# Kernel tuning notes

Hardware: AMD Instinct MI355X
Metric: run time of the kernel (lower is better)

The kernel has to match this reference:

```python
import jax, jax.numpy as jnp
import numpy as np

P_DIMS = [512, 256, 128]
K_DIMS = [256, 256, 256]
NT = 65536


def setup_inputs() -> dict:
    key = jax.random.key(0)
    ks = jax.random.split(key, 8 * len(P_DIMS))
    inp = {}
    ki = 0
    for i, (p, k) in enumerate(zip(P_DIMS, K_DIMS)):
        inp[f"x{i}"] = jax.random.normal(ks[ki], (NT, p), jnp.float32); ki += 1
        inp[f"alpha{i}"] = jax.random.normal(ks[ki], (1, k), jnp.float32); ki += 1
        inp[f"beta{i}"] = jax.random.normal(ks[ki], (k, p), jnp.float32) * 0.05; ki += 1
        inp[f"sig{i}"] = jax.random.normal(ks[ki], (1, k), jnp.float32); ki += 1
        inp[f"eta{i}"] = jax.random.normal(ks[ki], (1, k), jnp.float32); ki += 1
        inp[f"gam{i}"] = jax.random.normal(ks[ki], (k, 1), jnp.float32) * 0.03; ki += 1
        inp[f"w{i}"] = jax.random.normal(ks[ki], (k, p), jnp.float32); ki += 1
        inp[f"disc{i}"] = jnp.array([3.0], jnp.float32); ki += 1
    return inp


def _source(x, alpha, beta, sig, eta, gam, w, disc):
    # x: (nt,p); w,beta: (k,p); alpha,sig,eta: (1,k); gam: (k,1); disc: (1,)
    h = eta ** 2                                           # (1,k)
    d2 = (jnp.sum(x * x, axis=1, keepdims=True)
          - 2.0 * (x @ w.T)
          + jnp.sum(w * w, axis=1)[None, :])
    a = jnp.exp(-(gam[:, 0] ** 2)[None, :] * d2)           # (nt,k)
    ah = a * h                                             # a * H
    hx = jnp.sum(ah, axis=1)                               # (nt,)
    mu = x @ beta.T + alpha                                # (nt,k)
    mux = jnp.sum(mu * ah, axis=1) / hx
    sig2x = jnp.sum((sig ** 2) * (ah ** 2), axis=1) / (hx * hx)
    hx_dc = hx * jax.nn.sigmoid(disc[0])
    return mux, sig2x, hx, hx_dc


def reference(x0, alpha0, beta0, sig0, eta0, gam0, w0, disc0,
              x1, alpha1, beta1, sig1, eta1, gam1, w1, disc1,
              x2, alpha2, beta2, sig2, eta2, gam2, w2, disc2):
    srcs = [
        (x0, alpha0, beta0, sig0, eta0, gam0, w0, disc0),
        (x1, alpha1, beta1, sig1, eta1, gam1, w1, disc1),
        (x2, alpha2, beta2, sig2, eta2, gam2, w2, disc2),
    ]
    outs = [_source(*s) for s in srcs]  # fixed small loop over sources
    mux_t = jnp.stack([o[0] for o in outs])     # (S,nt)
    sig2x_t = jnp.stack([o[1] for o in outs])
    hx_t = jnp.stack([o[2] for o in outs])
    hx_dc = jnp.stack([o[3] for o in outs])
    denom = jnp.sum(hx_dc, axis=0)
    mux_comb = jnp.sum(mux_t * hx_dc, axis=0) / denom
    sig2x_comb = jnp.sum(sig2x_t * hx_dc ** 2, axis=0) / (denom ** 2)
    mux_final = jnp.concatenate([mux_t, mux_comb[None]], axis=0)      # (S+1,nt)
    sig2x_final = jnp.concatenate([sig2x_t, sig2x_comb[None]], axis=0)
    hx_final = jnp.concatenate([hx_t, denom[None]], axis=0)
    return (mux_final, sig2x_final, hx_final)
```

## Files before the change

kernel.cpp:

```cpp
#include <hip/hip_runtime.h>
#include <hip/hip_bf16.h>

typedef __attribute__((ext_vector_type(8))) short short8;
typedef __attribute__((ext_vector_type(4))) float f32x4;

#define NT 65536

__device__ __forceinline__ unsigned short f2bf(float f) {
    union { float f; unsigned int u; } v; v.f = f;
    unsigned int u = v.u;
    unsigned int r = (u + 0x7fffu + ((u >> 16) & 1u)) >> 16;
    return (unsigned short)r;
}

__device__ __forceinline__ unsigned int cvt_pk_bf16(float lo, float hi) {
    unsigned int r;
    asm("v_cvt_pk_bf16_f32 %0, %1, %2" : "=v"(r) : "v"(lo), "v"(hi));
    return r;
}

__global__ void prep_kernel(const float* __restrict__ w, const float* __restrict__ beta,
                            const float* __restrict__ alpha, const float* __restrict__ sig,
                            const float* __restrict__ eta, const float* __restrict__ gam,
                            unsigned short* __restrict__ bc, float* __restrict__ prm, int P) {
    __shared__ float red[2];
    const int n = blockIdx.x;
    const int tid = threadIdx.x;
    const int wb = n >> 5;
    const int j = n & 31;
    const bool isw = (j < 16);
    const int k = wb * 16 + (j & 15);
    const float* src = (isw ? w : beta) + (size_t)k * P;
    unsigned short* dst = bc + (size_t)n * P;
    float ss = 0.f;
    for (int c = tid; c < P; c += 128) {
        float f = src[c];
        dst[c] = f2bf(f);
        if (isw) ss += f * f;
    }
#pragma unroll
    for (int m = 1; m < 64; m <<= 1) ss += __shfl_xor(ss, m);
    if ((tid & 63) == 0) red[tid >> 6] = ss;
    __syncthreads();
    if (isw && tid == 0) prm[k] = red[0] + red[1];
    if (n == 0) {
        for (int kk = tid; kk < 256; kk += 128) {
            float g = gam[kk], e = eta[kk];
            prm[256 + kk]  = g * g;
            prm[512 + kk]  = e * e;
            prm[768 + kk]  = alpha[kk];
            prm[1024 + kk] = sig[kk] * sig[kk];
        }
    }
}

template<int P>
__global__ __launch_bounds__(512, 2)
void fused_src(const float* __restrict__ x, const unsigned short* __restrict__ Bc,
               const float* __restrict__ prm, float* __restrict__ pws) {
    constexpr int KS  = P / 32;
    constexpr int IST = P / 64;
    constexpr int WIN = (P == 256) ? 4 : 2;
    __shared__ unsigned short As[2][64 * P];
    __shared__ float part[8][64][3];
    __shared__ float xn2s[2][64];

    const int bx = blockIdx.x;
    const int h  = bx & 1;
    const int rg = bx >> 1;
    const int tid = threadIdx.x, lane = tid & 63, wv = tid >> 6;
    const int l15 = lane & 15, l4 = lane >> 4;
    const int wb = h * 8 + wv;

    short8 Bf[2][KS];
#pragma unroll
    for (int st = 0; st < 2; st++)
#pragma unroll
        for (int ks = 0; ks < KS; ks++)
            Bf[st][ks] = *(const short8*)(Bc + (size_t)(wb * 32 + st * 16 + l15) * P + ks * 32 + l4 * 8);

    const int kb = wb * 16 + 4 * l4;
    const f32x4 wn2 = *(const f32x4*)(prm + kb);
    const f32x4 g2  = *(const f32x4*)(prm + 256 + kb);
    const f32x4 hv  = *(const f32x4*)(prm + 512 + kb);
    const f32x4 alv = *(const f32x4*)(prm + 768 + kb);
    const f32x4 s2v = *(const f32x4*)(prm + 1024 + kb);

    float* pw = pws + (size_t)h * 3 * NT;

    const int srow = tid >> 3;
    const int ssl0 = tid & 7;

    {
        const int row0 = rg * 64;
        float4 pa[IST], pb[IST];
#pragma unroll
        for (int i = 0; i < IST; i++) {
            const float* gp = x + (size_t)(row0 + srow) * P + (ssl0 + 8 * i) * 8;
            pa[i] = *(const float4*)(gp);
            pb[i] = *(const float4*)(gp + 4);
        }
        float ssacc = 0.f;
#pragma unroll
        for (int i = 0; i < IST; i++) {
            float4 a0 = pa[i], a1 = pb[i];
            ssacc += a0.x*a0.x + a0.y*a0.y + a0.z*a0.z + a0.w*a0.w
                   + a1.x*a1.x + a1.y*a1.y + a1.z*a1.z + a1.w*a1.w;
            uint4 pk = { cvt_pk_bf16(a0.x, a0.y), cvt_pk_bf16(a0.z, a0.w),
                         cvt_pk_bf16(a1.x, a1.y), cvt_pk_bf16(a1.z, a1.w) };
            const int slot = ssl0 + 8 * i;
            *(uint4*)(&As[0][srow * P + ((slot ^ (srow & 7)) << 3)]) = pk;
        }
        ssacc += __shfl_xor(ssacc, 1);
        ssacc += __shfl_xor(ssacc, 2);
        ssacc += __shfl_xor(ssacc, 4);
        if (ssl0 == 0) xn2s[0][srow] = ssacc;
    }
    __syncthreads();

    int buf = 0;
    for (int tt = 0; tt < 8; tt++) {
        const int tile = rg + 128 * tt;
        const int row0 = tile * 64;
        const bool more = (tt < 7);
        const int nrow0 = (tile + 128) * 64;

        f32x4 acc[2][4];
#pragma unroll
        for (int st = 0; st < 2; st++)
#pragma unroll
            for (int rf = 0; rf < 4; rf++) acc[st][rf] = (f32x4){0.f, 0.f, 0.f, 0.f};

        float4 gfa[WIN], gfb[WIN];
        float ssacc = 0.f;

#pragma unroll
        for (int ks = 0; ks < KS; ks++) {
            if (more && ks >= WIN && (ks - WIN) < IST) {
                const int i = ks - WIN;
                float4 a0 = gfa[i % WIN], a1 = gfb[i % WIN];
                ssacc += a0.x*a0.x + a0.y*a0.y + a0.z*a0.z + a0.w*a0.w
                       + a1.x*a1.x + a1.y*a1.y + a1.z*a1.z + a1.w*a1.w;
                uint4 pk = { cvt_pk_bf16(a0.x, a0.y), cvt_pk_bf16(a0.z, a0.w),
                             cvt_pk_bf16(a1.x, a1.y), cvt_pk_bf16(a1.z, a1.w) };
                const int slot = ssl0 + 8 * i;
                *(uint4*)(&As[buf ^ 1][srow * P + ((slot ^ (srow & 7)) << 3)]) = pk;
            }
            if (more && ks < IST) {
                const float* gp = x + (size_t)(nrow0 + srow) * P + (ssl0 + 8 * ks) * 8;
                gfa[ks % WIN] = *(const float4*)(gp);
                gfb[ks % WIN] = *(const float4*)(gp + 4);
            }
            short8 af[4];
#pragma unroll
            for (int rf = 0; rf < 4; rf++) {
                const int row = 16 * rf + l15;
                af[rf] = *(const short8*)(&As[buf][row * P + (((ks * 4 + l4) ^ (row & 7)) << 3)]);
            }
#pragma unroll
            for (int rf = 0; rf < 4; rf++) {
                acc[0][rf] = __builtin_amdgcn_mfma_f32_16x16x32_bf16(Bf[0][ks], af[rf], acc[0][rf], 0, 0, 0);
                acc[1][rf] = __builtin_amdgcn_mfma_f32_16x16x32_bf16(Bf[1][ks], af[rf], acc[1][rf], 0, 0, 0);
            }
        }

        if (more) {
            ssacc += __shfl_xor(ssacc, 1);
            ssacc += __shfl_xor(ssacc, 2);
            ssacc += __shfl_xor(ssacc, 4);
            if (ssl0 == 0) xn2s[buf ^ 1][srow] = ssacc;
        }

#pragma unroll
        for (int rf = 0; rf < 4; rf++) {
            const int row = 16 * rf + l15;
            const float xv = xn2s[buf][row];
            float hs = 0.f, ms = 0.f, gs = 0.f;
#pragma unroll
            for (int j = 0; j < 4; j++) {
                float d2 = xv - 2.f * acc[0][rf][j] + wn2[j];
                float a  = __expf(-g2[j] * d2);
                float ah = a * hv[j];
                hs += ah;
                ms += (acc[1][rf][j] + alv[j]) * ah;
                gs += s2v[j] * ah * ah;
            }
            hs += __shfl_xor(hs, 16); hs += __shfl_xor(hs, 32);
            ms += __shfl_xor(ms, 16); ms += __shfl_xor(ms, 32);
            gs += __shfl_xor(gs, 16); gs += __shfl_xor(gs, 32);
            if (l4 == 0) { part[wv][row][0] = hs; part[wv][row][1] = ms; part[wv][row][2] = gs; }
        }
        __syncthreads();
        if (tid < 192) {
            const int v = tid >> 6, r = tid & 63;
            float sum = 0.f;
#pragma unroll
            for (int w8 = 0; w8 < 8; w8++) sum += part[w8][r][v];
            pw[(size_t)v * NT + row0 + r] = sum;
        }
        __syncthreads();
        buf ^= 1;
    }
}

__global__ void combine_kernel(const float* __restrict__ pws,
                               const float* __restrict__ d0, const float* __restrict__ d1,
                               const float* __restrict__ d2, float* __restrict__ out) {
    const int t = blockIdx.x * 256 + threadIdx.x;
    float mux[3], s2x[3], hx[3];
#pragma unroll
    for (int s = 0; s < 3; s++) {
        const float* b = pws + (size_t)s * 6 * NT;
        const float hh = b[t] + b[(size_t)3 * NT + t];
        const float mm = b[(size_t)1 * NT + t] + b[(size_t)4 * NT + t];
        const float gg = b[(size_t)2 * NT + t] + b[(size_t)5 * NT + t];
        mux[s] = mm / hh; s2x[s] = gg / (hh * hh); hx[s] = hh;
        out[(size_t)s * NT + t]       = mux[s];
        out[(size_t)(4 + s) * NT + t] = s2x[s];
        out[(size_t)(8 + s) * NT + t] = hh;
    }
    const float sd0 = 1.f / (1.f + __expf(-d0[0]));
    const float sd1 = 1.f / (1.f + __expf(-d1[0]));
    const float sd2 = 1.f / (1.f + __expf(-d2[0]));
    const float c0 = hx[0] * sd0, c1 = hx[1] * sd1, c2 = hx[2] * sd2;
    const float den = c0 + c1 + c2;
    const float muc = mux[0] * c0 + mux[1] * c1 + mux[2] * c2;
    const float sgc = s2x[0] * c0 * c0 + s2x[1] * c1 * c1 + s2x[2] * c2 * c2;
    out[(size_t)3 * NT + t]  = muc / den;
    out[(size_t)7 * NT + t]  = sgc / (den * den);
    out[(size_t)11 * NT + t] = den;
}

extern "C" void kernel_launch(void* const* d_in, const int* in_sizes, int n_in,
                              void* d_out, int out_size, void* d_ws, size_t ws_size,
                              hipStream_t stream) {
    const float* x0 = (const float*)d_in[0];
    const float* x1 = (const float*)d_in[8];
    const float* x2 = (const float*)d_in[16];

    unsigned short* bc = (unsigned short*)d_ws;
    float* prmAll = (float*)((char*)d_ws + 917504);
    float* pws    = (float*)((char*)d_ws + 917504 + 15360);
    float* out = (float*)d_out;

    const int Ps[3] = {512, 256, 128};
    const size_t bcoff[3] = {0, 512 * 512, 512 * 512 + 512 * 256};
    for (int s = 0; s < 3; s++) {
        prep_kernel<<<512, 128, 0, stream>>>((const float*)d_in[8 * s + 6], (const float*)d_in[8 * s + 2],
                                             (const float*)d_in[8 * s + 1], (const float*)d_in[8 * s + 3],
                                             (const float*)d_in[8 * s + 4], (const float*)d_in[8 * s + 5],
                                             bc + bcoff[s], prmAll + s * 1280, Ps[s]);
    }
    fused_src<512><<<256, 512, 0, stream>>>(x0, bc + bcoff[0], prmAll,          pws);
    fused_src<256><<<256, 512, 0, stream>>>(x1, bc + bcoff[1], prmAll + 1280,   pws + (size_t)6 * NT);
    fused_src<128><<<256, 512, 0, stream>>>(x2, bc + bcoff[2], prmAll + 2560,   pws + (size_t)12 * NT);
    combine_kernel<<<256, 256, 0, stream>>>(pws, (const float*)d_in[7], (const float*)d_in[15],
                                            (const float*)d_in[23], out);
}
```

Measured before the change: 133.9 us.

## Split P=512 reduction across wave pairs and widen k-split to four groups

For the P=512 source, each k-group of 16 columns is now handled by two waves, each covering half the reduction dimension. The two partial accumulators are summed through an LDS exchange that reuses the current A buffer. This halves the per-wave B fragment registers for P=512, and blocks are split four ways over k instead of two, giving more tiles per block with fewer row groups. The combine kernel now sums a variable number of partial groups per source. In exchange there is an extra barrier and LDS round-trip per tile, and half the waves sit idle during the epilogue.

New measurement: 149.5 us. 11.6% more time.

```diff
diff --git a/kernel.cpp b/kernel.cpp
--- a/kernel.cpp
+++ b/kernel.cpp
@@ -26,10 +26,10 @@
     __shared__ float red[2];
     const int n = blockIdx.x;
     const int tid = threadIdx.x;
-    const int wb = n >> 5;
-    const int j = n & 31;
-    const bool isw = (j < 16);
-    const int k = wb * 16 + (j & 15);
+    const int k16 = n >> 5;
+    const int typ = (n >> 4) & 1;
+    const int k = k16 * 16 + (n & 15);
+    const bool isw = (typ == 0);
     const float* src = (isw ? w : beta) + (size_t)k * P;
     unsigned short* dst = bc + (size_t)n * P;
     float ss = 0.f;
@@ -58,52 +58,55 @@
 __global__ __launch_bounds__(512, 2)
 void fused_src(const float* __restrict__ x, const unsigned short* __restrict__ Bc,
                const float* __restrict__ prm, float* __restrict__ pws) {
-    constexpr int KS  = P / 32;
-    constexpr int IST = P / 64;
-    constexpr int WIN = (P == 256) ? 4 : 2;
+    constexpr int  KSPLIT = (P == 512) ? 4 : 2;
+    constexpr bool PPS    = (P == 512);
+    constexpr int  KSW    = PPS ? P / 64 : P / 32;
+    constexpr int  IST    = P / 64;
+    constexpr int  WIN    = (IST < 4) ? IST : 4;
+    constexpr int  NRG    = 256 / KSPLIT;
+    constexpr int  T      = 1024 / NRG;
+
     __shared__ unsigned short As[2][64 * P];
+    __shared__ float xn2s[2][64];
     __shared__ float part[8][64][3];
-    __shared__ float xn2s[2][64];
 
     const int bx = blockIdx.x;
-    const int h  = bx & 1;
-    const int rg = bx >> 1;
+    const int h  = bx / NRG;
+    const int rg = bx % NRG;
     const int tid = threadIdx.x, lane = tid & 63, wv = tid >> 6;
     const int l15 = lane & 15, l4 = lane >> 4;
-    const int wb = h * 8 + wv;
-
-    short8 Bf[2][KS];
-#pragma unroll
-    for (int st = 0; st < 2; st++)
-#pragma unroll
-        for (int ks = 0; ks < KS; ks++)
-            Bf[st][ks] = *(const short8*)(Bc + (size_t)(wb * 32 + st * 16 + l15) * P + ks * 32 + l4 * 8);
-
-    const int kb = wb * 16 + 4 * l4;
+
+    int k16, pp, kset;
+    if (PPS) { kset = wv >> 1; pp = wv & 1; k16 = h * 4 + kset; }
+    else     { kset = wv;      pp = 0;      k16 = h * 8 + wv; }
+    const int ppoff = PPS ? pp * (P / 2) : 0;
+
+    short8 Bf[2][KSW];
+#pragma unroll
+    for (int typ = 0; typ < 2; typ++)
+#pragma unroll
+        for (int ks = 0; ks < KSW; ks++)
+            Bf[typ][ks] = *(const short8*)(Bc + (size_t)(k16 * 32 + typ * 16 + l15) * P
+                                           + ppoff + ks * 32 + l4 * 8);
+
+    const int kb = k16 * 16 + 4 * l4;
     const f32x4 wn2 = *(const f32x4*)(prm + kb);
     const f32x4 g2  = *(const f32x4*)(prm + 256 + kb);
     const f32x4 hv  = *(const f32x4*)(prm + 512 + kb);
     const f32x4 alv = *(const f32x4*)(prm + 768 + kb);
     const f32x4 s2v = *(const f32x4*)(prm + 1024 + kb);
 
-    float* pw = pws + (size_t)h * 3 * NT;
-
     const int srow = tid >> 3;
     const int ssl0 = tid & 7;
 
     {
         const int row0 = rg * 64;
-        float4 pa[IST], pb[IST];
+        float ssacc = 0.f;
 #pragma unroll
         for (int i = 0; i < IST; i++) {
             const float* gp = x + (size_t)(row0 + srow) * P + (ssl0 + 8 * i) * 8;
-            pa[i] = *(const float4*)(gp);
-            pb[i] = *(const float4*)(gp + 4);
-        }
-        float ssacc = 0.f;
-#pragma unroll
-        for (int i = 0; i < IST; i++) {
-            float4 a0 = pa[i], a1 = pb[i];
+            float4 a0 = *(const float4*)(gp);
+            float4 a1 = *(const float4*)(gp + 4);
             ssacc += a0.x*a0.x + a0.y*a0.y + a0.z*a0.z + a0.w*a0.w
                    + a1.x*a1.x + a1.y*a1.y + a1.z*a1.z + a1.w*a1.w;
             uint4 pk = { cvt_pk_bf16(a0.x, a0.y), cvt_pk_bf16(a0.z, a0.w),
@@ -119,28 +122,27 @@
     __syncthreads();
 
     int buf = 0;
-    for (int tt = 0; tt < 8; tt++) {
-        const int tile = rg + 128 * tt;
-        const int row0 = tile * 64;
-        const bool more = (tt < 7);
-        const int nrow0 = (tile + 128) * 64;
+    for (int tt = 0; tt < T; tt++) {
+        const int row0 = (rg + NRG * tt) * 64;
+        const bool more = (tt < T - 1);
+        const int nrow0 = (rg + NRG * (tt + 1)) * 64;
 
         f32x4 acc[2][4];
 #pragma unroll
-        for (int st = 0; st < 2; st++)
-#pragma unroll
-            for (int rf = 0; rf < 4; rf++) acc[st][rf] = (f32x4){0.f, 0.f, 0.f, 0.f};
-
-        float4 gfa[WIN], gfb[WIN];
-        float ssacc = 0.f;
-
-#pragma unroll
-        for (int ks = 0; ks < KS; ks++) {
+        for (int typ = 0; typ < 2; typ++)
+#pragma unroll
+            for (int rf = 0; rf < 4; rf++) acc[typ][rf] = (f32x4){0.f, 0.f, 0.f, 0.f};
+
+        float4 ga[WIN], gb[WIN];
+        float ssn = 0.f;
+
+#pragma unroll
+        for (int ks = 0; ks < KSW; ks++) {
             if (more && ks >= WIN && (ks - WIN) < IST) {
                 const int i = ks - WIN;
-                float4 a0 = gfa[i % WIN], a1 = gfb[i % WIN];
-                ssacc += a0.x*a0.x + a0.y*a0.y + a0.z*a0.z + a0.w*a0.w
-                       + a1.x*a1.x + a1.y*a1.y + a1.z*a1.z + a1.w*a1.w;
+                float4 a0 = ga[i % WIN], a1 = gb[i % WIN];
+                ssn += a0.x*a0.x + a0.y*a0.y + a0.z*a0.z + a0.w*a0.w
+                     + a1.x*a1.x + a1.y*a1.y + a1.z*a1.z + a1.w*a1.w;
                 uint4 pk = { cvt_pk_bf16(a0.x, a0.y), cvt_pk_bf16(a0.z, a0.w),
                              cvt_pk_bf16(a1.x, a1.y), cvt_pk_bf16(a1.z, a1.w) };
                 const int slot = ssl0 + 8 * i;
@@ -148,14 +150,15 @@
             }
             if (more && ks < IST) {
                 const float* gp = x + (size_t)(nrow0 + srow) * P + (ssl0 + 8 * ks) * 8;
-                gfa[ks % WIN] = *(const float4*)(gp);
-                gfb[ks % WIN] = *(const float4*)(gp + 4);
+                ga[ks % WIN] = *(const float4*)(gp);
+                gb[ks % WIN] = *(const float4*)(gp + 4);
             }
             short8 af[4];
 #pragma unroll
             for (int rf = 0; rf < 4; rf++) {
                 const int row = 16 * rf + l15;
-                af[rf] = *(const short8*)(&As[buf][row * P + (((ks * 4 + l4) ^ (row & 7)) << 3)]);
+                const int slotIdx = (ppoff >> 3) + ks * 4 + l4;
+                af[rf] = *(const short8*)(&As[buf][row * P + ((slotIdx ^ (row & 7)) << 3)]);
             }
 #pragma unroll
             for (int rf = 0; rf < 4; rf++) {
@@ -165,40 +168,75 @@
         }
 
         if (more) {
-            ssacc += __shfl_xor(ssacc, 1);
-            ssacc += __shfl_xor(ssacc, 2);
-            ssacc += __shfl_xor(ssacc, 4);
-            if (ssl0 == 0) xn2s[buf ^ 1][srow] = ssacc;
-        }
-
-#pragma unroll
-        for (int rf = 0; rf < 4; rf++) {
-            const int row = 16 * rf + l15;
-            const float xv = xn2s[buf][row];
-            float hs = 0.f, ms = 0.f, gs = 0.f;
-#pragma unroll
-            for (int j = 0; j < 4; j++) {
-                float d2 = xv - 2.f * acc[0][rf][j] + wn2[j];
-                float a  = __expf(-g2[j] * d2);
-                float ah = a * hv[j];
-                hs += ah;
-                ms += (acc[1][rf][j] + alv[j]) * ah;
-                gs += s2v[j] * ah * ah;
-            }
-            hs += __shfl_xor(hs, 16); hs += __shfl_xor(hs, 32);
-            ms += __shfl_xor(ms, 16); ms += __shfl_xor(ms, 32);
-            gs += __shfl_xor(gs, 16); gs += __shfl_xor(gs, 32);
-            if (l4 == 0) { part[wv][row][0] = hs; part[wv][row][1] = ms; part[wv][row][2] = gs; }
+#pragma unroll
+            for (int i = (KSW - WIN < 0 ? 0 : KSW - WIN); i < IST; i++) {
+                float4 a0 = ga[i % WIN], a1 = gb[i % WIN];
+                ssn += a0.x*a0.x + a0.y*a0.y + a0.z*a0.z + a0.w*a0.w
+                     + a1.x*a1.x + a1.y*a1.y + a1.z*a1.z + a1.w*a1.w;
+                uint4 pk = { cvt_pk_bf16(a0.x, a0.y), cvt_pk_bf16(a0.z, a0.w),
+                             cvt_pk_bf16(a1.x, a1.y), cvt_pk_bf16(a1.z, a1.w) };
+                const int slot = ssl0 + 8 * i;
+                *(uint4*)(&As[buf ^ 1][srow * P + ((slot ^ (srow & 7)) << 3)]) = pk;
+            }
+            ssn += __shfl_xor(ssn, 1);
+            ssn += __shfl_xor(ssn, 2);
+            ssn += __shfl_xor(ssn, 4);
+            if (ssl0 == 0) xn2s[buf ^ 1][srow] = ssn;
         }
         __syncthreads();
+
+        if constexpr (PPS) {
+            f32x4* exch = (f32x4*)&As[buf][0];
+            if (pp == 1) {
+#pragma unroll
+                for (int typ = 0; typ < 2; typ++)
+#pragma unroll
+                    for (int rf = 0; rf < 4; rf++)
+                        exch[((kset * 2 + typ) * 4 + rf) * 64 + lane] = acc[typ][rf];
+            }
+            __syncthreads();
+            if (pp == 0) {
+#pragma unroll
+                for (int typ = 0; typ < 2; typ++)
+#pragma unroll
+                    for (int rf = 0; rf < 4; rf++) {
+                        f32x4 o = exch[((kset * 2 + typ) * 4 + rf) * 64 + lane];
+                        acc[typ][rf] += o;
+                    }
+            }
+        }
+
+        if (!PPS || pp == 0) {
+#pragma unroll
+            for (int rf = 0; rf < 4; rf++) {
+                const int row = 16 * rf + l15;
+                const float xv = xn2s[buf][row];
+                float hs = 0.f, ms = 0.f, gs = 0.f;
+#pragma unroll
+                for (int j = 0; j < 4; j++) {
+                    float d2 = xv - 2.f * acc[0][rf][j] + wn2[j];
+                    float a  = __expf(-g2[j] * d2);
+                    float ah = a * hv[j];
+                    hs += ah;
+                    ms += (acc[1][rf][j] + alv[j]) * ah;
+                    gs += s2v[j] * ah * ah;
+                }
+                hs += __shfl_xor(hs, 16); hs += __shfl_xor(hs, 32);
+                ms += __shfl_xor(ms, 16); ms += __shfl_xor(ms, 32);
+                gs += __shfl_xor(gs, 16); gs += __shfl_xor(gs, 32);
+                if (l4 == 0) { part[kset][row][0] = hs; part[kset][row][1] = ms; part[kset][row][2] = gs; }
+            }
+        }
+        __syncthreads();
+
         if (tid < 192) {
+            constexpr int NG = PPS ? 4 : 8;
             const int v = tid >> 6, r = tid & 63;
             float sum = 0.f;
 #pragma unroll
-            for (int w8 = 0; w8 < 8; w8++) sum += part[w8][r][v];
-            pw[(size_t)v * NT + row0 + r] = sum;
-        }
-        __syncthreads();
+            for (int g = 0; g < NG; g++) sum += part[g][r][v];
+            pws[(size_t)(h * 3 + v) * NT + row0 + r] = sum;
+        }
         buf ^= 1;
     }
 }
@@ -207,13 +245,18 @@
                                const float* __restrict__ d0, const float* __restrict__ d1,
                                const float* __restrict__ d2, float* __restrict__ out) {
     const int t = blockIdx.x * 256 + threadIdx.x;
+    const int ng[3]  = {4, 2, 2};
+    const int off[3] = {0, 12, 18};
     float mux[3], s2x[3], hx[3];
 #pragma unroll
     for (int s = 0; s < 3; s++) {
-        const float* b = pws + (size_t)s * 6 * NT;
-        const float hh = b[t] + b[(size_t)3 * NT + t];
-        const float mm = b[(size_t)1 * NT + t] + b[(size_t)4 * NT + t];
-        const float gg = b[(size_t)2 * NT + t] + b[(size_t)5 * NT + t];
+        const float* b = pws + (size_t)off[s] * NT;
+        float hh = 0.f, mm = 0.f, gg = 0.f;
+        for (int g = 0; g < ng[s]; g++) {
+            hh += b[(size_t)(g * 3 + 0) * NT + t];
+            mm += b[(size_t)(g * 3 + 1) * NT + t];
+            gg += b[(size_t)(g * 3 + 2) * NT + t];
+        }
         mux[s] = mm / hh; s2x[s] = gg / (hh * hh); hx[s] = hh;
         out[(size_t)s * NT + t]       = mux[s];
         out[(size_t)(4 + s) * NT + t] = s2x[s];
@@ -251,9 +294,9 @@
                                              (const float*)d_in[8 * s + 4], (const float*)d_in[8 * s + 5],
                                              bc + bcoff[s], prmAll + s * 1280, Ps[s]);
     }
-    fused_src<512><<<256, 512, 0, stream>>>(x0, bc + bcoff[0], prmAll,          pws);
-    fused_src<256><<<256, 512, 0, stream>>>(x1, bc + bcoff[1], prmAll + 1280,   pws + (size_t)6 * NT);
-    fused_src<128><<<256, 512, 0, stream>>>(x2, bc + bcoff[2], prmAll + 2560,   pws + (size_t)12 * NT);
+    fused_src<512><<<256, 512, 0, stream>>>(x0, bc + bcoff[0], prmAll,        pws);
+    fused_src<256><<<256, 512, 0, stream>>>(x1, bc + bcoff[1], prmAll + 1280, pws + (size_t)12 * NT);
+    fused_src<128><<<256, 512, 0, stream>>>(x2, bc + bcoff[2], prmAll + 2560, pws + (size_t)18 * NT);
     combine_kernel<<<256, 256, 0, stream>>>(pws, (const float*)d_in[7], (const float*)d_in[15],
                                             (const float*)d_in[23], out);
 }
```

## Fuse per-source launches into single 256x256-tile kernel with LDS-staged weights

Applied to the files above, without the earlier changes.

Merges the three prep launches and the three per-source GEMM launches into one launch each, indexing the source by block ID. The main kernel switches from register-resident weight fragments with 64-row tiles to 256x256 output tiles with a K loop. Weights stream into double-buffered LDS via global_load_lds, while x is converted to bf16 in registers. The aim is to raise data reuse per tile and cut launch overhead and serialisation between sources. In exchange it needs about 150KB of LDS and a large accumulator, so only one block fits per CU, and the sources with shorter K have few loop iterations to overlap loads with compute.

After: 181.8 us. 1.36x slower.

```diff
diff --git a/kernel.cpp b/kernel.cpp
--- a/kernel.cpp
+++ b/kernel.cpp
@@ -19,19 +19,42 @@
     return r;
 }
 
-__global__ void prep_kernel(const float* __restrict__ w, const float* __restrict__ beta,
-                            const float* __restrict__ alpha, const float* __restrict__ sig,
-                            const float* __restrict__ eta, const float* __restrict__ gam,
-                            unsigned short* __restrict__ bc, float* __restrict__ prm, int P) {
+#define LGKM0() asm volatile("s_waitcnt lgkmcnt(0)" ::: "memory")
+#define VMC0()  asm volatile("s_waitcnt vmcnt(0)" ::: "memory")
+#define BAR()   __builtin_amdgcn_s_barrier()
+#define SB0()   __builtin_amdgcn_sched_barrier(0)
+
+__global__ void prep_kernel(const float* __restrict__ w0, const float* __restrict__ b0,
+                            const float* __restrict__ a0, const float* __restrict__ s0,
+                            const float* __restrict__ e0, const float* __restrict__ g0,
+                            const float* __restrict__ w1, const float* __restrict__ b1,
+                            const float* __restrict__ a1, const float* __restrict__ s1,
+                            const float* __restrict__ e1, const float* __restrict__ g1,
+                            const float* __restrict__ w2, const float* __restrict__ b2,
+                            const float* __restrict__ a2, const float* __restrict__ s2,
+                            const float* __restrict__ e2, const float* __restrict__ g2,
+                            unsigned short* __restrict__ bc, float* __restrict__ prmAll) {
     __shared__ float red[2];
-    const int n = blockIdx.x;
+    const int bx = blockIdx.x;
+    const int s = bx >> 9;
+    const int n = bx & 511;
+    const int P = 512 >> s;
+    const float* w   = (s == 0) ? w0 : ((s == 1) ? w1 : w2);
+    const float* bet = (s == 0) ? b0 : ((s == 1) ? b1 : b2);
+    const float* alp = (s == 0) ? a0 : ((s == 1) ? a1 : a2);
+    const float* sig = (s == 0) ? s0 : ((s == 1) ? s1 : s2);
+    const float* eta = (s == 0) ? e0 : ((s == 1) ? e1 : e2);
+    const float* gam = (s == 0) ? g0 : ((s == 1) ? g1 : g2);
+    unsigned short* dstb = bc + ((s == 0) ? 0 : ((s == 1) ? (512 * 512) : (512 * 512 + 512 * 256)));
+    float* prm = prmAll + 1280 * s;
+
     const int tid = threadIdx.x;
-    const int wb = n >> 5;
-    const int j = n & 31;
-    const bool isw = (j < 16);
-    const int k = wb * 16 + (j & 15);
-    const float* src = (isw ? w : beta) + (size_t)k * P;
-    unsigned short* dst = bc + (size_t)n * P;
+    const int k16 = n >> 5;
+    const int typ = (n >> 4) & 1;
+    const int k = k16 * 16 + (n & 15);
+    const bool isw = (typ == 0);
+    const float* src = (isw ? w : bet) + (size_t)k * P;
+    unsigned short* dst = dstb + (size_t)n * P;
     float ss = 0.f;
     for (int c = tid; c < P; c += 128) {
         float f = src[c];
@@ -48,158 +71,171 @@
             float g = gam[kk], e = eta[kk];
             prm[256 + kk]  = g * g;
             prm[512 + kk]  = e * e;
-            prm[768 + kk]  = alpha[kk];
+            prm[768 + kk]  = alp[kk];
             prm[1024 + kk] = sig[kk] * sig[kk];
         }
     }
 }
 
-template<int P>
 __global__ __launch_bounds__(512, 2)
-void fused_src(const float* __restrict__ x, const unsigned short* __restrict__ Bc,
-               const float* __restrict__ prm, float* __restrict__ pws) {
-    constexpr int KS  = P / 32;
-    constexpr int IST = P / 64;
-    constexpr int WIN = (P == 256) ? 4 : 2;
-    __shared__ unsigned short As[2][64 * P];
-    __shared__ float part[8][64][3];
-    __shared__ float xn2s[2][64];
+void fused_all(const float* __restrict__ x0, const float* __restrict__ x1, const float* __restrict__ x2,
+               const unsigned short* __restrict__ bcAll, const float* __restrict__ prmAll,
+               float* __restrict__ pws) {
+    __shared__ unsigned short Ab[2][256 * 72];
+    __shared__ unsigned short Bb[2][256 * 64];
+    __shared__ float xn2[256];
+    __shared__ float part[4][256][3];
 
     const int bx = blockIdx.x;
-    const int h  = bx & 1;
-    const int rg = bx >> 1;
+    const int s  = bx >> 9;
+    const int local = bx & 511;
+    const int mt = local & 255;
+    const int h  = local >> 8;
+    const int P  = 512 >> s;
+    const int NK = P >> 6;
+    const float* x = (s == 0) ? x0 : ((s == 1) ? x1 : x2);
+    const unsigned short* Bc = bcAll + ((s == 0) ? 0 : ((s == 1) ? (512 * 512) : (512 * 512 + 512 * 256)));
+    const float* prm = prmAll + 1280 * s;
+    float* pw = pws + (size_t)(s * 6 + h * 3) * NT;
+    const int row0 = mt * 256;
+
     const int tid = threadIdx.x, lane = tid & 63, wv = tid >> 6;
+    const int wr = wv >> 2, wcn = wv & 3;
     const int l15 = lane & 15, l4 = lane >> 4;
-    const int wb = h * 8 + wv;
-
-    short8 Bf[2][KS];
-#pragma unroll
-    for (int st = 0; st < 2; st++)
-#pragma unroll
-        for (int ks = 0; ks < KS; ks++)
-            Bf[st][ks] = *(const short8*)(Bc + (size_t)(wb * 32 + st * 16 + l15) * P + ks * 32 + l4 * 8);
-
-    const int kb = wb * 16 + 4 * l4;
-    const f32x4 wn2 = *(const f32x4*)(prm + kb);
-    const f32x4 g2  = *(const f32x4*)(prm + 256 + kb);
-    const f32x4 hv  = *(const f32x4*)(prm + 512 + kb);
-    const f32x4 alv = *(const f32x4*)(prm + 768 + kb);
-    const f32x4 s2v = *(const f32x4*)(prm + 1024 + kb);
-
-    float* pw = pws + (size_t)h * 3 * NT;
-
-    const int srow = tid >> 3;
-    const int ssl0 = tid & 7;
-
-    {
-        const int row0 = rg * 64;
-        float4 pa[IST], pb[IST];
-#pragma unroll
-        for (int i = 0; i < IST; i++) {
-            const float* gp = x + (size_t)(row0 + srow) * P + (ssl0 + 8 * i) * 8;
-            pa[i] = *(const float4*)(gp);
-            pb[i] = *(const float4*)(gp + 4);
-        }
-        float ssacc = 0.f;
-#pragma unroll
-        for (int i = 0; i < IST; i++) {
-            float4 a0 = pa[i], a1 = pb[i];
-            ssacc += a0.x*a0.x + a0.y*a0.y + a0.z*a0.z + a0.w*a0.w
-                   + a1.x*a1.x + a1.y*a1.y + a1.z*a1.z + a1.w*a1.w;
-            uint4 pk = { cvt_pk_bf16(a0.x, a0.y), cvt_pk_bf16(a0.z, a0.w),
-                         cvt_pk_bf16(a1.x, a1.y), cvt_pk_bf16(a1.z, a1.w) };
-            const int slot = ssl0 + 8 * i;
-            *(uint4*)(&As[0][srow * P + ((slot ^ (srow & 7)) << 3)]) = pk;
-        }
-        ssacc += __shfl_xor(ssacc, 1);
-        ssacc += __shfl_xor(ssacc, 2);
-        ssacc += __shfl_xor(ssacc, 4);
-        if (ssl0 == 0) xn2s[0][srow] = ssacc;
-    }
+
+    const int arow = tid >> 1, ahalf = tid & 1;
+    const float* xrow = x + (size_t)(row0 + arow) * P + ahalf * 32;
+
+    const int brr = tid >> 3;
+    const int bslot = (tid & 7) ^ (brr & 7);
+
+    f32x4 acc[8][4];
+#pragma unroll
+    for (int rf = 0; rf < 8; rf++)
+#pragma unroll
+        for (int cf = 0; cf < 4; cf++) acc[rf][cf] = (f32x4){0.f, 0.f, 0.f, 0.f};
+
+    float ss = 0.f;
+    float4 ar[8];
+
+    auto stage_B = [&](int nb, int t) {
+#pragma unroll
+        for (int i = 0; i < 4; i++) {
+            const unsigned short* src = Bc + (size_t)(256 * h + i * 64 + brr) * P + t * 64 + bslot * 8;
+            __builtin_amdgcn_global_load_lds((const __attribute__((address_space(1))) void*)src,
+                                             (__attribute__((address_space(3))) void*)&Bb[nb][(i * 512 + wv * 64) * 8],
+                                             16, 0, 0);
+        }
+    };
+    auto load_A = [&](int t) {
+#pragma unroll
+        for (int i = 0; i < 8; i++) ar[i] = *(const float4*)(xrow + t * 64 + i * 4);
+    };
+    auto cvt_write_A = [&](int nb) {
+#pragma unroll
+        for (int i2 = 0; i2 < 4; i2++) {
+            float4 q0 = ar[2 * i2], q1 = ar[2 * i2 + 1];
+            ss += q0.x*q0.x + q0.y*q0.y + q0.z*q0.z + q0.w*q0.w
+                + q1.x*q1.x + q1.y*q1.y + q1.z*q1.z + q1.w*q1.w;
+            uint4 pk = { cvt_pk_bf16(q0.x, q0.y), cvt_pk_bf16(q0.z, q0.w),
+                         cvt_pk_bf16(q1.x, q1.y), cvt_pk_bf16(q1.z, q1.w) };
+            *(uint4*)(&Ab[nb][arow * 72 + (ahalf * 4 + i2) * 8]) = pk;
+        }
+    };
+    auto compute = [&](int buf) {
+#pragma unroll
+        for (int kk = 0; kk < 2; kk++) {
+            short8 bfr[4];
+#pragma unroll
+            for (int cf = 0; cf < 4; cf++) {
+                const int rowb = wcn * 64 + cf * 16 + l15;
+                bfr[cf] = *(const short8*)(&Bb[buf][rowb * 64 + (((kk * 4 + l4) ^ (rowb & 7)) << 3)]);
+            }
+#pragma unroll
+            for (int rf = 0; rf < 8; rf++) {
+                const int rowa = wr * 128 + rf * 16 + l15;
+                short8 af = *(const short8*)(&Ab[buf][rowa * 72 + (kk * 4 + l4) * 8]);
+#pragma unroll
+                for (int cf = 0; cf < 4; cf++)
+                    acc[rf][cf] = __builtin_amdgcn_mfma_f32_16x16x32_bf16(af, bfr[cf], acc[rf][cf], 0, 0, 0);
+            }
+        }
+    };
+
+    stage_B(0, 0);
+    SB0();
+    load_A(0);
+    SB0();
+    cvt_write_A(0);
+    VMC0(); LGKM0(); BAR(); SB0();
+
+#pragma unroll 1
+    for (int t = 0; t < NK - 1; t++) {
+        const int buf = t & 1;
+        stage_B(buf ^ 1, t + 1);
+        SB0();
+        load_A(t + 1);
+        SB0();
+        compute(buf);
+        SB0();
+        cvt_write_A(buf ^ 1);
+        LGKM0(); BAR(); SB0();
+    }
+    compute((NK - 1) & 1);
+    VMC0(); LGKM0(); BAR(); SB0();
+
+    ss += __shfl_xor(ss, 1);
+    if (ahalf == 0) xn2[arow] = ss;
     __syncthreads();
 
-    int buf = 0;
-    for (int tt = 0; tt < 8; tt++) {
-        const int tile = rg + 128 * tt;
-        const int row0 = tile * 64;
-        const bool more = (tt < 7);
-        const int nrow0 = (tile + 128) * 64;
-
-        f32x4 acc[2][4];
-#pragma unroll
-        for (int st = 0; st < 2; st++)
-#pragma unroll
-            for (int rf = 0; rf < 4; rf++) acc[st][rf] = (f32x4){0.f, 0.f, 0.f, 0.f};
-
-        float4 gfa[WIN], gfb[WIN];
-        float ssacc = 0.f;
-
-#pragma unroll
-        for (int ks = 0; ks < KS; ks++) {
-            if (more && ks >= WIN && (ks - WIN) < IST) {
-                const int i = ks - WIN;
-                float4 a0 = gfa[i % WIN], a1 = gfb[i % WIN];
-                ssacc += a0.x*a0.x + a0.y*a0.y + a0.z*a0.z + a0.w*a0.w
-                       + a1.x*a1.x + a1.y*a1.y + a1.z*a1.z + a1.w*a1.w;
-                uint4 pk = { cvt_pk_bf16(a0.x, a0.y), cvt_pk_bf16(a0.z, a0.w),
-                             cvt_pk_bf16(a1.x, a1.y), cvt_pk_bf16(a1.z, a1.w) };
-                const int slot = ssl0 + 8 * i;
-                *(uint4*)(&As[buf ^ 1][srow * P + ((slot ^ (srow & 7)) << 3)]) = pk;
-            }
-            if (more && ks < IST) {
-                const float* gp = x + (size_t)(nrow0 + srow) * P + (ssl0 + 8 * ks) * 8;
-                gfa[ks % WIN] = *(const float4*)(gp);
-                gfb[ks % WIN] = *(const float4*)(gp + 4);
-            }
-            short8 af[4];
-#pragma unroll
-            for (int rf = 0; rf < 4; rf++) {
-                const int row = 16 * rf + l15;
-                af[rf] = *(const short8*)(&As[buf][row * P + (((ks * 4 + l4) ^ (row & 7)) << 3)]);
-            }
-#pragma unroll
-            for (int rf = 0; rf < 4; rf++) {
-                acc[0][rf] = __builtin_amdgcn_mfma_f32_16x16x32_bf16(Bf[0][ks], af[rf], acc[0][rf], 0, 0, 0);
-                acc[1][rf] = __builtin_amdgcn_mfma_f32_16x16x32_bf16(Bf[1][ks], af[rf], acc[1][rf], 0, 0, 0);
-            }
-        }
-
-        if (more) {
-            ssacc += __shfl_xor(ssacc, 1);
-            ssacc += __shfl_xor(ssacc, 2);
-            ssacc += __shfl_xor(ssacc, 4);
-            if (ssl0 == 0) xn2s[buf ^ 1][srow] = ssacc;
-        }
-
-#pragma unroll
-        for (int rf = 0; rf < 4; rf++) {
-            const int row = 16 * rf + l15;
-            const float xv = xn2s[buf][row];
+    float wn2q[2], g2q[2], hvq[2], alq[2], s2q[2];
+#pragma unroll
+    for (int q = 0; q < 2; q++) {
+        const int k = (8 * h + 2 * wcn + q) * 16 + l15;
+        wn2q[q] = prm[k];
+        g2q[q]  = prm[256 + k];
+        hvq[q]  = prm[512 + k];
+        alq[q]  = prm[768 + k];
+        s2q[q]  = prm[1024 + k];
+    }
+#pragma unroll
+    for (int rf = 0; rf < 8; rf++) {
+#pragma unroll
+        for (int j = 0; j < 4; j++) {
+            const int row = wr * 128 + rf * 16 + l4 * 4 + j;
+            const float xv = xn2[row];
             float hs = 0.f, ms = 0.f, gs = 0.f;
 #pragma unroll
-            for (int j = 0; j < 4; j++) {
-                float d2 = xv - 2.f * acc[0][rf][j] + wn2[j];
-                float a  = __expf(-g2[j] * d2);
-                float ah = a * hv[j];
+            for (int q = 0; q < 2; q++) {
+                const float aw = acc[rf][2 * q][j];
+                const float ab2 = acc[rf][2 * q + 1][j];
+                const float d2 = xv - 2.f * aw + wn2q[q];
+                const float a  = __expf(-g2q[q] * d2);
+                const float ah = a * hvq[q];
                 hs += ah;
-                ms += (acc[1][rf][j] + alv[j]) * ah;
-                gs += s2v[j] * ah * ah;
-            }
-            hs += __shfl_xor(hs, 16); hs += __shfl_xor(hs, 32);
-            ms += __shfl_xor(ms, 16); ms += __shfl_xor(ms, 32);
-            gs += __shfl_xor(gs, 16); gs += __shfl_xor(gs, 32);
-            if (l4 == 0) { part[wv][row][0] = hs; part[wv][row][1] = ms; part[wv][row][2] = gs; }
-        }
-        __syncthreads();
-        if (tid < 192) {
-            const int v = tid >> 6, r = tid & 63;
-            float sum = 0.f;
-#pragma unroll
-            for (int w8 = 0; w8 < 8; w8++) sum += part[w8][r][v];
-            pw[(size_t)v * NT + row0 + r] = sum;
-        }
-        __syncthreads();
-        buf ^= 1;
+                ms += (ab2 + alq[q]) * ah;
+                gs += s2q[q] * ah * ah;
+            }
+#pragma unroll
+            for (int msk = 1; msk < 16; msk <<= 1) {
+                hs += __shfl_xor(hs, msk);
+                ms += __shfl_xor(ms, msk);
+                gs += __shfl_xor(gs, msk);
+            }
+            if (l15 == 0) {
+                part[wcn][row][0] = hs;
+                part[wcn][row][1] = ms;
+                part[wcn][row][2] = gs;
+            }
+        }
+    }
+    __syncthreads();
+    if (tid < 256) {
+#pragma unroll
+        for (int v = 0; v < 3; v++) {
+            float sum = part[0][tid][v] + part[1][tid][v] + part[2][tid][v] + part[3][tid][v];
+            pw[(size_t)v * NT + row0 + tid] = sum;
+        }
     }
 }
 
@@ -243,17 +279,15 @@
     float* pws    = (float*)((char*)d_ws + 917504 + 15360);
     float* out = (float*)d_out;
 
-    const int Ps[3] = {512, 256, 128};
-    const size_t bcoff[3] = {0, 512 * 512, 512 * 512 + 512 * 256};
-    for (int s = 0; s < 3; s++) {
-        prep_kernel<<<512, 128, 0, stream>>>((const float*)d_in[8 * s + 6], (const float*)d_in[8 * s + 2],
-                                             (const float*)d_in[8 * s + 1], (const float*)d_in[8 * s + 3],
-                                             (const float*)d_in[8 * s + 4], (const float*)d_in[8 * s + 5],
-                                             bc + bcoff[s], prmAll + s * 1280, Ps[s]);
-    }
-    fused_src<512><<<256, 512, 0, stream>>>(x0, bc + bcoff[0], prmAll,          pws);
-    fused_src<256><<<256, 512, 0, stream>>>(x1, bc + bcoff[1], prmAll + 1280,   pws + (size_t)6 * NT);
-    fused_src<128><<<256, 512, 0, stream>>>(x2, bc + bcoff[2], prmAll + 2560,   pws + (size_t)12 * NT);
+    prep_kernel<<<1536, 128, 0, stream>>>(
+        (const float*)d_in[6],  (const float*)d_in[2],  (const float*)d_in[1],
+        (const float*)d_in[3],  (const float*)d_in[4],  (const float*)d_in[5],
+        (const float*)d_in[14], (const float*)d_in[10], (const float*)d_in[9],
+        (const float*)d_in[11], (const float*)d_in[12], (const float*)d_in[13],
+        (const float*)d_in[22], (const float*)d_in[18], (const float*)d_in[17],
+        (const float*)d_in[19], (const float*)d_in[20], (const float*)d_in[21],
+        bc, prmAll);
+    fused_all<<<1536, 512, 0, stream>>>(x0, x1, x2, bc, prmAll, pws);
     combine_kernel<<<256, 256, 0, stream>>>(pws, (const float*)d_in[7], (const float*)d_in[15],
                                             (const float*)d_in[23], out);
 }
```

## Merge per-source prep and GEMM kernels into single launches interleaving sources

Applied to the files above, without the earlier changes.

Merges the three prep launches into one 1536-block launch and the three per-source fused GEMM/exp kernels into one 768-block kernel. Block index modulo three selects the source, so all sources run concurrently and the serial launch chain and tail gaps go away. The shared buffer is now sized for the largest P (128KB of LDS for the A tiles), which limits residency to one block per CU (launch bounds 512,1). The pipeline also gains an extra drain loop for the remaining prefetched stages and an additional barrier per tile.

After: 145.2 us. +8.4%, slower.

```diff
diff --git a/kernel.cpp b/kernel.cpp
--- a/kernel.cpp
+++ b/kernel.cpp
@@ -19,19 +19,37 @@
     return r;
 }
 
-__global__ void prep_kernel(const float* __restrict__ w, const float* __restrict__ beta,
-                            const float* __restrict__ alpha, const float* __restrict__ sig,
-                            const float* __restrict__ eta, const float* __restrict__ gam,
-                            unsigned short* __restrict__ bc, float* __restrict__ prm, int P) {
+__global__ void prep_kernel(const float* __restrict__ w0, const float* __restrict__ b0,
+                            const float* __restrict__ a0, const float* __restrict__ s0,
+                            const float* __restrict__ e0, const float* __restrict__ g0,
+                            const float* __restrict__ w1, const float* __restrict__ b1,
+                            const float* __restrict__ a1, const float* __restrict__ s1,
+                            const float* __restrict__ e1, const float* __restrict__ g1,
+                            const float* __restrict__ w2, const float* __restrict__ b2,
+                            const float* __restrict__ a2, const float* __restrict__ s2,
+                            const float* __restrict__ e2, const float* __restrict__ g2,
+                            unsigned short* __restrict__ bc, float* __restrict__ prmAll) {
     __shared__ float red[2];
-    const int n = blockIdx.x;
+    const int bx = blockIdx.x;
+    const int s = bx >> 9;
+    const int n = bx & 511;
+    const int P = 512 >> s;
+    const float* w   = (s == 0) ? w0 : ((s == 1) ? w1 : w2);
+    const float* bet = (s == 0) ? b0 : ((s == 1) ? b1 : b2);
+    const float* alp = (s == 0) ? a0 : ((s == 1) ? a1 : a2);
+    const float* sig = (s == 0) ? s0 : ((s == 1) ? s1 : s2);
+    const float* eta = (s == 0) ? e0 : ((s == 1) ? e1 : e2);
+    const float* gam = (s == 0) ? g0 : ((s == 1) ? g1 : g2);
+    unsigned short* dstb = bc + ((s == 0) ? 0 : ((s == 1) ? (512 * 512) : (512 * 512 + 512 * 256)));
+    float* prm = prmAll + 1280 * s;
+
     const int tid = threadIdx.x;
-    const int wb = n >> 5;
-    const int j = n & 31;
-    const bool isw = (j < 16);
-    const int k = wb * 16 + (j & 15);
-    const float* src = (isw ? w : beta) + (size_t)k * P;
-    unsigned short* dst = bc + (size_t)n * P;
+    const int k16 = n >> 5;
+    const int typ = (n >> 4) & 1;
+    const int k = k16 * 16 + (n & 15);
+    const bool isw = (typ == 0);
+    const float* src = (isw ? w : bet) + (size_t)k * P;
+    unsigned short* dst = dstb + (size_t)n * P;
     float ss = 0.f;
     for (int c = tid; c < P; c += 128) {
         float f = src[c];
@@ -48,45 +66,40 @@
             float g = gam[kk], e = eta[kk];
             prm[256 + kk]  = g * g;
             prm[512 + kk]  = e * e;
-            prm[768 + kk]  = alpha[kk];
+            prm[768 + kk]  = alp[kk];
             prm[1024 + kk] = sig[kk] * sig[kk];
         }
     }
 }
 
 template<int P>
-__global__ __launch_bounds__(512, 2)
-void fused_src(const float* __restrict__ x, const unsigned short* __restrict__ Bc,
-               const float* __restrict__ prm, float* __restrict__ pws) {
+__device__ __forceinline__ void body(const float* __restrict__ x,
+                                     const unsigned short* __restrict__ Bc,
+                                     const float* __restrict__ prm,
+                                     float* __restrict__ pws, int h, int rg,
+                                     unsigned short* AsU, float (*xn2s)[64],
+                                     float (*part)[64][3], int tid) {
     constexpr int KS  = P / 32;
     constexpr int IST = P / 64;
     constexpr int WIN = (P == 256) ? 4 : 2;
-    __shared__ unsigned short As[2][64 * P];
-    __shared__ float part[8][64][3];
-    __shared__ float xn2s[2][64];
-
-    const int bx = blockIdx.x;
-    const int h  = bx & 1;
-    const int rg = bx >> 1;
-    const int tid = threadIdx.x, lane = tid & 63, wv = tid >> 6;
+
+    const int lane = tid & 63, wv = tid >> 6;
     const int l15 = lane & 15, l4 = lane >> 4;
-    const int wb = h * 8 + wv;
+    const int k16 = h * 8 + wv;
 
     short8 Bf[2][KS];
 #pragma unroll
     for (int st = 0; st < 2; st++)
 #pragma unroll
         for (int ks = 0; ks < KS; ks++)
-            Bf[st][ks] = *(const short8*)(Bc + (size_t)(wb * 32 + st * 16 + l15) * P + ks * 32 + l4 * 8);
-
-    const int kb = wb * 16 + 4 * l4;
+            Bf[st][ks] = *(const short8*)(Bc + (size_t)(k16 * 32 + st * 16 + l15) * P + ks * 32 + l4 * 8);
+
+    const int kb = k16 * 16 + 4 * l4;
     const f32x4 wn2 = *(const f32x4*)(prm + kb);
     const f32x4 g2  = *(const f32x4*)(prm + 256 + kb);
     const f32x4 hv  = *(const f32x4*)(prm + 512 + kb);
     const f32x4 alv = *(const f32x4*)(prm + 768 + kb);
     const f32x4 s2v = *(const f32x4*)(prm + 1024 + kb);
-
-    float* pw = pws + (size_t)h * 3 * NT;
 
     const int srow = tid >> 3;
     const int ssl0 = tid & 7;
@@ -109,7 +122,7 @@
             uint4 pk = { cvt_pk_bf16(a0.x, a0.y), cvt_pk_bf16(a0.z, a0.w),
                          cvt_pk_bf16(a1.x, a1.y), cvt_pk_bf16(a1.z, a1.w) };
             const int slot = ssl0 + 8 * i;
-            *(uint4*)(&As[0][srow * P + ((slot ^ (srow & 7)) << 3)]) = pk;
+            *(uint4*)(AsU + srow * P + ((slot ^ (srow & 7)) << 3)) = pk;
         }
         ssacc += __shfl_xor(ssacc, 1);
         ssacc += __shfl_xor(ssacc, 2);
@@ -144,7 +157,7 @@
                 uint4 pk = { cvt_pk_bf16(a0.x, a0.y), cvt_pk_bf16(a0.z, a0.w),
                              cvt_pk_bf16(a1.x, a1.y), cvt_pk_bf16(a1.z, a1.w) };
                 const int slot = ssl0 + 8 * i;
-                *(uint4*)(&As[buf ^ 1][srow * P + ((slot ^ (srow & 7)) << 3)]) = pk;
+                *(uint4*)(AsU + (buf ^ 1) * 64 * P + srow * P + ((slot ^ (srow & 7)) << 3)) = pk;
             }
             if (more && ks < IST) {
                 const float* gp = x + (size_t)(nrow0 + srow) * P + (ssl0 + 8 * ks) * 8;
@@ -155,7 +168,7 @@
 #pragma unroll
             for (int rf = 0; rf < 4; rf++) {
                 const int row = 16 * rf + l15;
-                af[rf] = *(const short8*)(&As[buf][row * P + (((ks * 4 + l4) ^ (row & 7)) << 3)]);
+                af[rf] = *(const short8*)(AsU + buf * 64 * P + row * P + (((ks * 4 + l4) ^ (row & 7)) << 3));
             }
 #pragma unroll
             for (int rf = 0; rf < 4; rf++) {
@@ -165,11 +178,22 @@
         }
 
         if (more) {
+#pragma unroll
+            for (int i = (KS - WIN < 0 ? 0 : KS - WIN); i < IST; i++) {
+                float4 a0 = gfa[i % WIN], a1 = gfb[i % WIN];
+                ssacc += a0.x*a0.x + a0.y*a0.y + a0.z*a0.z + a0.w*a0.w
+                       + a1.x*a1.x + a1.y*a1.y + a1.z*a1.z + a1.w*a1.w;
+                uint4 pk = { cvt_pk_bf16(a0.x, a0.y), cvt_pk_bf16(a0.z, a0.w),
+                             cvt_pk_bf16(a1.x, a1.y), cvt_pk_bf16(a1.z, a1.w) };
+                const int slot = ssl0 + 8 * i;
+                *(uint4*)(AsU + (buf ^ 1) * 64 * P + srow * P + ((slot ^ (srow & 7)) << 3)) = pk;
+            }
             ssacc += __shfl_xor(ssacc, 1);
             ssacc += __shfl_xor(ssacc, 2);
             ssacc += __shfl_xor(ssacc, 4);
             if (ssl0 == 0) xn2s[buf ^ 1][srow] = ssacc;
         }
+        __syncthreads();
 
 #pragma unroll
         for (int rf = 0; rf < 4; rf++) {
@@ -196,11 +220,36 @@
             float sum = 0.f;
 #pragma unroll
             for (int w8 = 0; w8 < 8; w8++) sum += part[w8][r][v];
-            pw[(size_t)v * NT + row0 + r] = sum;
+            pws[(size_t)(h * 3 + v) * NT + row0 + r] = sum;
         }
         __syncthreads();
         buf ^= 1;
     }
+}
+
+__global__ __launch_bounds__(512, 1)
+void fused_all(const float* __restrict__ x0, const float* __restrict__ x1, const float* __restrict__ x2,
+               const unsigned short* __restrict__ bcAll, const float* __restrict__ prmAll,
+               float* __restrict__ pws) {
+    __shared__ unsigned short As[2][64 * 512];
+    __shared__ float part[8][64][3];
+    __shared__ float xn2s[2][64];
+
+    const int bx = blockIdx.x;
+    const int src = bx % 3;
+    const int local = bx / 3;
+    const int h = local & 1;
+    const int rg = local >> 1;
+    const int tid = threadIdx.x;
+
+    if (src == 0)
+        body<512>(x0, bcAll, prmAll, pws, h, rg, &As[0][0], xn2s, part, tid);
+    else if (src == 1)
+        body<256>(x1, bcAll + 512 * 512, prmAll + 1280, pws + (size_t)6 * NT,
+                  h, rg, &As[0][0], xn2s, part, tid);
+    else
+        body<128>(x2, bcAll + 512 * 512 + 512 * 256, prmAll + 2560, pws + (size_t)12 * NT,
+                  h, rg, &As[0][0], xn2s, part, tid);
 }
 
 __global__ void combine_kernel(const float* __restrict__ pws,
@@ -243,17 +292,16 @@
     float* pws    = (float*)((char*)d_ws + 917504 + 15360);
     float* out = (float*)d_out;
 
-    const int Ps[3] = {512, 256, 128};
-    const size_t bcoff[3] = {0, 512 * 512, 512 * 512 + 512 * 256};
-    for (int s = 0; s < 3; s++) {
-        prep_kernel<<<512, 128, 0, stream>>>((const float*)d_in[8 * s + 6], (const float*)d_in[8 * s + 2],
-                                             (const float*)d_in[8 * s + 1], (const float*)d_in[8 * s + 3],
-                                             (const float*)d_in[8 * s + 4], (const float*)d_in[8 * s + 5],
-                                             bc + bcoff[s], prmAll + s * 1280, Ps[s]);
-    }
-    fused_src<512><<<256, 512, 0, stream>>>(x0, bc + bcoff[0], prmAll,          pws);
-    fused_src<256><<<256, 512, 0, stream>>>(x1, bc + bcoff[1], prmAll + 1280,   pws + (size_t)6 * NT);
-    fused_src<128><<<256, 512, 0, stream>>>(x2, bc + bcoff[2], prmAll + 2560,   pws + (size_t)12 * NT);
+    prep_kernel<<<1536, 128, 0, stream>>>(
+        (const float*)d_in[6],  (const float*)d_in[2],  (const float*)d_in[1],
+        (const float*)d_in[3],  (const float*)d_in[4],  (const float*)d_in[5],
+        (const float*)d_in[14], (const float*)d_in[10], (const float*)d_in[9],
+        (const float*)d_in[11], (const float*)d_in[12], (const float*)d_in[13],
+        (const float*)d_in[22], (const float*)d_in[18], (const float*)d_in[17],
+        (const float*)d_in[19], (const float*)d_in[20], (const float*)d_in[21],
+        bc, prmAll);
+
+    fused_all<<<768, 512, 0, stream>>>(x0, x1, x2, bc, prmAll, pws);
     combine_kernel<<<256, 256, 0, stream>>>(pws, (const float*)d_in[7], (const float*)d_in[15],
                                             (const float*)d_in[23], out);
 }
```
